# Kernel optimization log

Measured on AMD Instinct MI355X. Metric: run time of the kernel, lower is better.

The kernel has to match this reference:

```python
import jax, jax.numpy as jnp
import numpy as np

HIDDEN = 1024
HEADS = 16
HEAD_DIM = HIDDEN // HEADS
LN_EPS = 1e-5


def setup_inputs() -> dict:
    key = jax.random.key(0)
    ks = jax.random.split(key, 8)
    B, S = 4, 2048
    s = 1.0 / np.sqrt(HIDDEN)
    return {
        "x": jax.random.normal(ks[0], (B, S, HIDDEN), dtype=jnp.float32),
        "Wq": jax.random.normal(ks[1], (HIDDEN, HIDDEN), dtype=jnp.float32) * s,
        "bq": jax.random.normal(ks[2], (HIDDEN,), dtype=jnp.float32) * 0.01,
        "Wk": jax.random.normal(ks[3], (HIDDEN, HIDDEN), dtype=jnp.float32) * s,
        "bk": jax.random.normal(ks[4], (HIDDEN,), dtype=jnp.float32) * 0.01,
        "Wv": jax.random.normal(ks[5], (HIDDEN, HIDDEN), dtype=jnp.float32) * s,
        "bv": jax.random.normal(ks[6], (HIDDEN,), dtype=jnp.float32) * 0.01,
        "gamma": jnp.ones((HIDDEN,), dtype=jnp.float32),
        "beta": jnp.zeros((HIDDEN,), dtype=jnp.float32),
    }


def reference(x, Wq, bq, Wk, bk, Wv, bv, gamma, beta):
    B, S, H = x.shape
    # LayerNorm
    mu = jnp.mean(x, axis=-1, keepdims=True)
    var = jnp.mean(jnp.square(x - mu), axis=-1, keepdims=True)
    xn = (x - mu) / jnp.sqrt(var + LN_EPS) * gamma + beta
    # QKV projections -> [B, heads, S, head_dim]
    def split_heads(t):
        return t.reshape(B, S, HEADS, HEAD_DIM).transpose(0, 2, 1, 3)
    q = split_heads(xn @ Wq + bq)
    k = split_heads(xn @ Wk + bk)
    v = split_heads(xn @ Wv + bv)
    scores = jnp.einsum("bhqd,bhkd->bhqk", q, k) / np.sqrt(HEAD_DIM)
    probs = jax.nn.softmax(scores, axis=-1)
    attended = jnp.einsum("bhqk,bhkd->bhqd", probs, v)
    attended = attended.transpose(0, 2, 1, 3).reshape(B, S, H)
    # residual (dropout = 0.0 / eval mode is identity)
    return xn + attended
```

## Files before the change

kernel.cpp:

```cpp
#include <hip/hip_runtime.h>
#include <hip/hip_bf16.h>

#define HIDDEN 1024
#define HEADS 16
#define HEAD_DIM 64
#define SEQ 2048
#define BATCH 4

typedef __attribute__((ext_vector_type(8))) short bf16x8;
typedef __attribute__((ext_vector_type(4))) float f32x4;
typedef __attribute__((ext_vector_type(16))) float f32x16;
typedef __attribute__((ext_vector_type(4))) short short4v;

static __device__ __forceinline__ unsigned short f2bf(float f) {
  union { float f; unsigned u; } u;
  u.f = f;
  unsigned r = u.u + 0x7fffu + ((u.u >> 16) & 1u);
  return (unsigned short)(r >> 16);
}

static __device__ __forceinline__ unsigned packtr(float lo, float hi) {
  union { float f; unsigned u; } a, b;
  a.f = lo; b.f = hi;
#if __has_builtin(__builtin_amdgcn_perm)
  return __builtin_amdgcn_perm(b.u, a.u, 0x07060302u);
#else
  return (b.u & 0xFFFF0000u) | (a.u >> 16);
#endif
}

static __device__ __forceinline__ bf16x8 frag4(unsigned u0, unsigned u1,
                                               unsigned u2, unsigned u3) {
  union { unsigned u[4]; bf16x8 v; } t;
  t.u[0] = u0; t.u[1] = u1; t.u[2] = u2; t.u[3] = u3;
  return t.v;
}

static __device__ __forceinline__ float fexp2(float x) {
#if __has_builtin(__builtin_amdgcn_exp2f)
  return __builtin_amdgcn_exp2f(x);
#else
  return exp2f(x);
#endif
}

typedef const __attribute__((address_space(1))) unsigned int* gp1_t;
typedef __attribute__((address_space(3))) unsigned int* lp3_t;
static __device__ __forceinline__ void gload_lds16(const void* g, void* l) {
  __builtin_amdgcn_global_load_lds((gp1_t)g, (lp3_t)l, 16, 0, 0);
}

__global__ __launch_bounds__(256) void wtrans_kernel(
    const float* __restrict__ Wq, const float* __restrict__ Wk,
    const float* __restrict__ Wv, unsigned short* __restrict__ Wt) {
  __shared__ float tile[64][65];
  int z = blockIdx.z;
  const float* W = (z == 0) ? Wq : (z == 1) ? Wk : Wv;
  int k0 = blockIdx.x * 64, n0 = blockIdx.y * 64;
  int tid = threadIdx.x;
  int tr = tid >> 4;
  int tc = tid & 15;
#pragma unroll
  for (int p = 0; p < 4; ++p) {
    int kk = p * 16 + tr;
    float4 v = *(const float4*)(W + (size_t)(k0 + kk) * HIDDEN + n0 + tc * 4);
    tile[kk][tc * 4 + 0] = v.x; tile[kk][tc * 4 + 1] = v.y;
    tile[kk][tc * 4 + 2] = v.z; tile[kk][tc * 4 + 3] = v.w;
  }
  __syncthreads();
  unsigned short* op = Wt + (size_t)z * HIDDEN * HIDDEN;
#pragma unroll
  for (int p = 0; p < 4; ++p) {
    int nn = p * 16 + tr;
    short4v o;
    o.x = (short)f2bf(tile[tc * 4 + 0][nn]);
    o.y = (short)f2bf(tile[tc * 4 + 1][nn]);
    o.z = (short)f2bf(tile[tc * 4 + 2][nn]);
    o.w = (short)f2bf(tile[tc * 4 + 3][nn]);
    *(short4v*)(op + (size_t)(n0 + nn) * HIDDEN + k0 + tc * 4) = o;
  }
}

__global__ __launch_bounds__(256) void ln_kernel(
    const float* __restrict__ x, const float* __restrict__ gamma,
    const float* __restrict__ beta, float* __restrict__ out,
    unsigned short* __restrict__ xnb) {
  int row = blockIdx.x;
  int tid = threadIdx.x;
  const float4* xr = (const float4*)(x + (size_t)row * HIDDEN);
  float4 v = xr[tid];
  float s = v.x + v.y + v.z + v.w;
  float sq = v.x * v.x + v.y * v.y + v.z * v.z + v.w * v.w;
#pragma unroll
  for (int off = 32; off >= 1; off >>= 1) {
    s += __shfl_xor(s, off);
    sq += __shfl_xor(sq, off);
  }
  __shared__ float red[8];
  int wave = tid >> 6, lane = tid & 63;
  if (lane == 0) { red[wave] = s; red[4 + wave] = sq; }
  __syncthreads();
  s = red[0] + red[1] + red[2] + red[3];
  sq = red[4] + red[5] + red[6] + red[7];
  float mu = s * (1.0f / HIDDEN);
  float var = sq * (1.0f / HIDDEN) - mu * mu;
  float rstd = rsqrtf(var + 1e-5f);
  float4 g = ((const float4*)gamma)[tid];
  float4 bt = ((const float4*)beta)[tid];
  float4 o;
  o.x = (v.x - mu) * rstd * g.x + bt.x;
  o.y = (v.y - mu) * rstd * g.y + bt.y;
  o.z = (v.z - mu) * rstd * g.z + bt.z;
  o.w = (v.w - mu) * rstd * g.w + bt.w;
  ((float4*)(out + (size_t)row * HIDDEN))[tid] = o;
  short4v p;
  p.x = (short)f2bf(o.x); p.y = (short)f2bf(o.y);
  p.z = (short)f2bf(o.z); p.w = (short)f2bf(o.w);
  *((short4v*)(xnb + (size_t)row * HIDDEN) + tid) = p;
}

__global__ __launch_bounds__(256) void qkv_gemm(
    const unsigned short* __restrict__ xnb, const unsigned short* __restrict__ Wt,
    const float* __restrict__ bq, const float* __restrict__ bk,
    const float* __restrict__ bv, unsigned short* __restrict__ qO,
    unsigned short* __restrict__ kO, unsigned short* __restrict__ vtO) {
  __shared__ unsigned short As[128 * 64];
  __shared__ unsigned short Bs[128 * 64];
  int z = blockIdx.z;
  int m0 = blockIdx.x * 128;
  int n0 = blockIdx.y * 128;
  int tid = threadIdx.x;
  int wave = tid >> 6, lane = tid & 63;
  int lr = lane & 15, g = lane >> 4;
  int wm = wave >> 1, wn = wave & 1;
  const unsigned short* Ab = xnb + (size_t)m0 * HIDDEN;
  const unsigned short* Bb = Wt + (size_t)z * HIDDEN * HIDDEN + (size_t)n0 * HIDDEN;
  int srow = wave * 8 + (lane >> 3);
  int scol = ((lane & 7) ^ (lane >> 3)) << 3;
  f32x4 acc[4][4];
#pragma unroll
  for (int i = 0; i < 4; ++i)
#pragma unroll
    for (int j = 0; j < 4; ++j) acc[i][j] = (f32x4){0.f, 0.f, 0.f, 0.f};

#pragma unroll 1
  for (int k0 = 0; k0 < HIDDEN; k0 += 64) {
#pragma unroll
    for (int i = 0; i < 4; ++i) {
      int row = i * 32 + srow;
      gload_lds16(Ab + (size_t)row * HIDDEN + k0 + scol, &As[(i * 32 + wave * 8) * 64]);
      gload_lds16(Bb + (size_t)row * HIDDEN + k0 + scol, &Bs[(i * 32 + wave * 8) * 64]);
    }
    __syncthreads();
    bf16x8 aF[4][2], bF[4][2];
#pragma unroll
    for (int mb = 0; mb < 4; ++mb) {
      int row = wm * 64 + mb * 16 + lr;
#pragma unroll
      for (int ks = 0; ks < 2; ++ks)
        aF[mb][ks] = *(const bf16x8*)&As[row * 64 + (((ks * 4 + g) ^ (row & 7)) << 3)];
    }
#pragma unroll
    for (int nb = 0; nb < 4; ++nb) {
      int row = wn * 64 + nb * 16 + lr;
#pragma unroll
      for (int ks = 0; ks < 2; ++ks)
        bF[nb][ks] = *(const bf16x8*)&Bs[row * 64 + (((ks * 4 + g) ^ (row & 7)) << 3)];
    }
#pragma unroll
    for (int ks = 0; ks < 2; ++ks)
#pragma unroll
      for (int mb = 0; mb < 4; ++mb)
#pragma unroll
        for (int nb = 0; nb < 4; ++nb)
          acc[mb][nb] = __builtin_amdgcn_mfma_f32_16x16x32_bf16(aF[mb][ks], bF[nb][ks], acc[mb][nb], 0, 0, 0);
    __syncthreads();
  }
  const float* bias = (z == 0) ? bq : (z == 1) ? bk : bv;
  if (z == 2) {
#pragma unroll
    for (int nb = 0; nb < 4; ++nb) {
      int n = n0 + wn * 64 + nb * 16 + lr;
      float bsv = bias[n];
      int h = n >> 6, d = n & 63;
#pragma unroll
      for (int mb = 0; mb < 4; ++mb) {
        int m = m0 + wm * 64 + mb * 16 + g * 4;
        int bb = m >> 11, sIdx = m & 2047;
        short4v pk;
        pk.x = (short)f2bf(acc[mb][nb][0] + bsv);
        pk.y = (short)f2bf(acc[mb][nb][1] + bsv);
        pk.z = (short)f2bf(acc[mb][nb][2] + bsv);
        pk.w = (short)f2bf(acc[mb][nb][3] + bsv);
        *(short4v*)(vtO + (size_t)((bb * HEADS + h) * HEAD_DIM + d) * SEQ + sIdx) = pk;
      }
    }
  } else {
    unsigned short* outp = (z == 0) ? qO : kO;
    float scale = (z == 0) ? 0.18033688011112042f : 1.0f;
#pragma unroll
    for (int nb = 0; nb < 4; ++nb) {
      int n = n0 + wn * 64 + nb * 16 + lr;
      float bsv = bias[n];
      int h = n >> 6, d = n & 63;
#pragma unroll
      for (int mb = 0; mb < 4; ++mb) {
#pragma unroll
        for (int r = 0; r < 4; ++r) {
          int m = m0 + wm * 64 + mb * 16 + g * 4 + r;
          int bb = m >> 11, sIdx = m & 2047;
          unsigned short bits = f2bf((acc[mb][nb][r] + bsv) * scale);
          outp[(size_t)((bb * HEADS + h) * SEQ + sIdx) * HEAD_DIM + d] = bits;
        }
      }
    }
  }
}

static __device__ __forceinline__ void attn_subtile(
    const unsigned short* __restrict__ Kb, const unsigned short* __restrict__ Vb,
    const int (&koff)[4], const bf16x8 (&qF)[4],
    const f32x16& ZERO, f32x16& o0, f32x16& o1, float& lsum) {
  f32x16 sc0, sc1;
  __builtin_amdgcn_s_setprio(1);
  {
    bf16x8 k0 = *(const bf16x8*)&Kb[koff[0]];
    bf16x8 k1 = *(const bf16x8*)&Kb[koff[0] + 2048];
    sc0 = __builtin_amdgcn_mfma_f32_32x32x16_bf16(k0, qF[0], ZERO, 0, 0, 0);
    sc1 = __builtin_amdgcn_mfma_f32_32x32x16_bf16(k1, qF[0], ZERO, 0, 0, 0);
  }
#pragma unroll
  for (int s = 1; s < 4; ++s) {
    bf16x8 k0 = *(const bf16x8*)&Kb[koff[s]];
    bf16x8 k1 = *(const bf16x8*)&Kb[koff[s] + 2048];
    sc0 = __builtin_amdgcn_mfma_f32_32x32x16_bf16(k0, qF[s], sc0, 0, 0, 0);
    sc1 = __builtin_amdgcn_mfma_f32_32x32x16_bf16(k1, qF[s], sc1, 0, 0, 0);
  }
  __builtin_amdgcn_s_setprio(0);
#pragma unroll
  for (int s = 0; s < 4; ++s) {
    float e[8];
#pragma unroll
    for (int j = 0; j < 8; ++j) {
      float scv = (s < 2) ? sc0[8 * s + j] : sc1[8 * (s - 2) + j];
      e[j] = fexp2(scv);
    }
    lsum += ((e[0] + e[1]) + (e[2] + e[3])) + ((e[4] + e[5]) + (e[6] + e[7]));
    unsigned pa0 = packtr(e[0], e[1]);
    unsigned pb0 = packtr(e[2], e[3]);
    unsigned pa1 = packtr(e[4], e[5]);
    unsigned pb1 = packtr(e[6], e[7]);
#if __has_builtin(__builtin_amdgcn_permlane32_swap)
    auto ra = __builtin_amdgcn_permlane32_swap(pa0, pa1, false, false);
    auto rb = __builtin_amdgcn_permlane32_swap(pb0, pb1, false, false);
    bf16x8 pF = frag4(ra[0], rb[0], ra[1], rb[1]);
#else
    int hf = (threadIdx.x & 63) >> 5;
    unsigned t0 = __shfl_xor(hf ? pa0 : pa1, 32);
    unsigned t1 = __shfl_xor(hf ? pb0 : pb1, 32);
    bf16x8 pF = frag4(hf ? t0 : pa0, hf ? t1 : pb0,
                      hf ? pa1 : t0, hf ? pb1 : t1);
#endif
    bf16x8 v0 = *(const bf16x8*)&Vb[koff[s]];
    bf16x8 v1 = *(const bf16x8*)&Vb[koff[s] + 2048];
    __builtin_amdgcn_s_setprio(1);
    o0 = __builtin_amdgcn_mfma_f32_32x32x16_bf16(v0, pF, o0, 0, 0, 0);
    o1 = __builtin_amdgcn_mfma_f32_32x32x16_bf16(v1, pF, o1, 0, 0, 0);
    __builtin_amdgcn_s_setprio(0);
  }
}

__global__ __launch_bounds__(512, 4) void attn_kernel(
    const unsigned short* __restrict__ qB, const unsigned short* __restrict__ kB,
    const unsigned short* __restrict__ vtB, float* __restrict__ out) {
  __shared__ unsigned short Kt[2][2][64 * 64];
  __shared__ unsigned short Vt[2][2][64 * 64];
  int orig = blockIdx.y * gridDim.x + blockIdx.x;
  int swz = (orig & 7) * 64 + (orig >> 3);
  int bx = swz & 7;
  int by = swz >> 3;
  int b = by >> 4, hh = by & 15;
  int tid = threadIdx.x, wave = tid >> 6, lane = tid & 63;
  int lq = lane & 31;
  int hf = lane >> 5;
  int q0 = bx * 256 + wave * 32;
  const unsigned short* qh = qB + (size_t)by * SEQ * HEAD_DIM;
  const unsigned short* kh = kB + (size_t)by * SEQ * HEAD_DIM;
  const unsigned short* vh = vtB + (size_t)by * HEAD_DIM * SEQ;

  bf16x8 qF[4];
#pragma unroll
  for (int s = 0; s < 4; ++s)
    qF[s] = *(const bf16x8*)(qh + (size_t)(q0 + lq) * HEAD_DIM + s * 16 + hf * 8);

  int srow = wave * 8 + (lane >> 3);
  int scoff = ((lane & 7) ^ (lane >> 3)) << 3;
  int xorb = (lq & 7) << 4;
  int koff[4];
#pragma unroll
  for (int s = 0; s < 4; ++s)
    koff[s] = (lq * 128 + ((s * 32 + hf * 16) ^ xorb)) >> 1;

  f32x16 o0, o1, ZERO;
#pragma unroll
  for (int r = 0; r < 16; ++r) { o0[r] = 0.f; o1[r] = 0.f; ZERO[r] = 0.f; }
  float lsum = 0.f;

#pragma unroll
  for (int sub = 0; sub < 2; ++sub) {
    gload_lds16(kh + (size_t)(sub * 64 + srow) * HEAD_DIM + scoff, &Kt[0][sub][wave * 512]);
    gload_lds16(vh + (size_t)srow * SEQ + sub * 64 + scoff, &Vt[0][sub][wave * 512]);
  }
  __syncthreads();

#pragma unroll 1
  for (int t = 0; t < 16; ++t) {
    int cur = t & 1;
    if (t < 15) {
      int kv1 = (t + 1) * 128;
#pragma unroll
      for (int sub = 0; sub < 2; ++sub) {
        gload_lds16(kh + (size_t)(kv1 + sub * 64 + srow) * HEAD_DIM + scoff,
                    &Kt[cur ^ 1][sub][wave * 512]);
        gload_lds16(vh + (size_t)srow * SEQ + kv1 + sub * 64 + scoff,
                    &Vt[cur ^ 1][sub][wave * 512]);
      }
    }
    attn_subtile(Kt[cur][0], Vt[cur][0], koff, qF, ZERO, o0, o1, lsum);
    attn_subtile(Kt[cur][1], Vt[cur][1], koff, qF, ZERO, o0, o1, lsum);
    __syncthreads();
  }
  lsum += __shfl_xor(lsum, 32);
  float inv = 1.0f / lsum;
  float* orow = out + ((size_t)b * SEQ + q0 + lq) * HIDDEN + hh * HEAD_DIM;
#pragma unroll
  for (int r = 0; r < 16; ++r) {
    int d0 = (r & 3) + 8 * (r >> 2) + 4 * hf;
    orow[d0] += o0[r] * inv;
    orow[32 + d0] += o1[r] * inv;
  }
}

extern "C" void kernel_launch(void* const* d_in, const int* in_sizes, int n_in,
                              void* d_out, int out_size, void* d_ws, size_t ws_size,
                              hipStream_t stream) {
  const float* x     = (const float*)d_in[0];
  const float* Wq    = (const float*)d_in[1];
  const float* bq    = (const float*)d_in[2];
  const float* Wk    = (const float*)d_in[3];
  const float* bk    = (const float*)d_in[4];
  const float* Wv    = (const float*)d_in[5];
  const float* bv    = (const float*)d_in[6];
  const float* gamma = (const float*)d_in[7];
  const float* beta  = (const float*)d_in[8];
  float* out = (float*)d_out;
  char* ws = (char*)d_ws;
  const size_t MB = 1024 * 1024;
  unsigned short* xnb = (unsigned short*)(ws);
  unsigned short* Wt  = (unsigned short*)(ws + 16 * MB);
  unsigned short* qb  = (unsigned short*)(ws + 22 * MB);
  unsigned short* kb  = (unsigned short*)(ws + 38 * MB);
  unsigned short* vtb = (unsigned short*)(ws + 54 * MB);

  hipLaunchKernelGGL(wtrans_kernel, dim3(16, 16, 3), dim3(256), 0, stream, Wq, Wk, Wv, Wt);
  hipLaunchKernelGGL(ln_kernel, dim3(BATCH * SEQ), dim3(256), 0, stream, x, gamma, beta, out, xnb);
  hipLaunchKernelGGL(qkv_gemm, dim3(64, 8, 3), dim3(256), 0, stream, xnb, Wt, bq, bk, bv, qb, kb, vtb);
  hipLaunchKernelGGL(attn_kernel, dim3(8, 64), dim3(512), 0, stream, qb, kb, vtb, out);
}
```

Baseline: 174.4 us.

## Double-buffer QKV GEMM tiles and re-layout attention K/V LDS tiles

The QKV GEMM now keeps two LDS buffers for the A and B tiles and prefetches the next k-slice while computing on the current one, so global loads can overlap with MFMA work. The attention kernel also changes how K and V tiles are staged into LDS: each wave loads an 8-element column chunk for all 64 rows, replacing the XOR-swizzled row layout, and fragment offsets are recomputed to match. The aim is fewer load stalls and simpler LDS addressing, at the cost of doubling GEMM LDS use, which may lower occupancy. The new attention global loads are more strided and may have different LDS bank-conflict behaviour.

```diff
diff --git a/kernel.cpp b/kernel.cpp
--- a/kernel.cpp
+++ b/kernel.cpp
@@ -124,8 +124,8 @@
     const float* __restrict__ bq, const float* __restrict__ bk,
     const float* __restrict__ bv, unsigned short* __restrict__ qO,
     unsigned short* __restrict__ kO, unsigned short* __restrict__ vtO) {
-  __shared__ unsigned short As[128 * 64];
-  __shared__ unsigned short Bs[128 * 64];
+  __shared__ unsigned short As[2][128 * 64];
+  __shared__ unsigned short Bs[2][128 * 64];
   int z = blockIdx.z;
   int m0 = blockIdx.x * 128;
   int n0 = blockIdx.y * 128;
@@ -143,29 +143,40 @@
 #pragma unroll
     for (int j = 0; j < 4; ++j) acc[i][j] = (f32x4){0.f, 0.f, 0.f, 0.f};
 
+#pragma unroll
+  for (int i = 0; i < 4; ++i) {
+    int row = i * 32 + srow;
+    gload_lds16(Ab + (size_t)row * HIDDEN + scol, &As[0][(i * 32 + wave * 8) * 64]);
+    gload_lds16(Bb + (size_t)row * HIDDEN + scol, &Bs[0][(i * 32 + wave * 8) * 64]);
+  }
+  __syncthreads();
+
 #pragma unroll 1
-  for (int k0 = 0; k0 < HIDDEN; k0 += 64) {
-#pragma unroll
-    for (int i = 0; i < 4; ++i) {
-      int row = i * 32 + srow;
-      gload_lds16(Ab + (size_t)row * HIDDEN + k0 + scol, &As[(i * 32 + wave * 8) * 64]);
-      gload_lds16(Bb + (size_t)row * HIDDEN + k0 + scol, &Bs[(i * 32 + wave * 8) * 64]);
-    }
-    __syncthreads();
+  for (int t = 0; t < 16; ++t) {
+    int cur = t & 1;
+    if (t < 15) {
+      int k1 = (t + 1) * 64;
+#pragma unroll
+      for (int i = 0; i < 4; ++i) {
+        int row = i * 32 + srow;
+        gload_lds16(Ab + (size_t)row * HIDDEN + k1 + scol, &As[cur ^ 1][(i * 32 + wave * 8) * 64]);
+        gload_lds16(Bb + (size_t)row * HIDDEN + k1 + scol, &Bs[cur ^ 1][(i * 32 + wave * 8) * 64]);
+      }
+    }
     bf16x8 aF[4][2], bF[4][2];
 #pragma unroll
     for (int mb = 0; mb < 4; ++mb) {
       int row = wm * 64 + mb * 16 + lr;
 #pragma unroll
       for (int ks = 0; ks < 2; ++ks)
-        aF[mb][ks] = *(const bf16x8*)&As[row * 64 + (((ks * 4 + g) ^ (row & 7)) << 3)];
+        aF[mb][ks] = *(const bf16x8*)&As[cur][row * 64 + (((ks * 4 + g) ^ (row & 7)) << 3)];
     }
 #pragma unroll
     for (int nb = 0; nb < 4; ++nb) {
       int row = wn * 64 + nb * 16 + lr;
 #pragma unroll
       for (int ks = 0; ks < 2; ++ks)
-        bF[nb][ks] = *(const bf16x8*)&Bs[row * 64 + (((ks * 4 + g) ^ (row & 7)) << 3)];
+        bF[nb][ks] = *(const bf16x8*)&Bs[cur][row * 64 + (((ks * 4 + g) ^ (row & 7)) << 3)];
     }
 #pragma unroll
     for (int ks = 0; ks < 2; ++ks)
@@ -225,14 +236,14 @@
   __builtin_amdgcn_s_setprio(1);
   {
     bf16x8 k0 = *(const bf16x8*)&Kb[koff[0]];
-    bf16x8 k1 = *(const bf16x8*)&Kb[koff[0] + 2048];
+    bf16x8 k1 = *(const bf16x8*)&Kb[koff[0] + 256];
     sc0 = __builtin_amdgcn_mfma_f32_32x32x16_bf16(k0, qF[0], ZERO, 0, 0, 0);
     sc1 = __builtin_amdgcn_mfma_f32_32x32x16_bf16(k1, qF[0], ZERO, 0, 0, 0);
   }
 #pragma unroll
   for (int s = 1; s < 4; ++s) {
     bf16x8 k0 = *(const bf16x8*)&Kb[koff[s]];
-    bf16x8 k1 = *(const bf16x8*)&Kb[koff[s] + 2048];
+    bf16x8 k1 = *(const bf16x8*)&Kb[koff[s] + 256];
     sc0 = __builtin_amdgcn_mfma_f32_32x32x16_bf16(k0, qF[s], sc0, 0, 0, 0);
     sc1 = __builtin_amdgcn_mfma_f32_32x32x16_bf16(k1, qF[s], sc1, 0, 0, 0);
   }
@@ -262,7 +273,7 @@
                       hf ? pa1 : t0, hf ? pb1 : t1);
 #endif
     bf16x8 v0 = *(const bf16x8*)&Vb[koff[s]];
-    bf16x8 v1 = *(const bf16x8*)&Vb[koff[s] + 2048];
+    bf16x8 v1 = *(const bf16x8*)&Vb[koff[s] + 256];
     __builtin_amdgcn_s_setprio(1);
     o0 = __builtin_amdgcn_mfma_f32_32x32x16_bf16(v0, pF, o0, 0, 0, 0);
     o1 = __builtin_amdgcn_mfma_f32_32x32x16_bf16(v1, pF, o1, 0, 0, 0);
@@ -293,13 +304,10 @@
   for (int s = 0; s < 4; ++s)
     qF[s] = *(const bf16x8*)(qh + (size_t)(q0 + lq) * HEAD_DIM + s * 16 + hf * 8);
 
-  int srow = wave * 8 + (lane >> 3);
-  int scoff = ((lane & 7) ^ (lane >> 3)) << 3;
-  int xorb = (lq & 7) << 4;
   int koff[4];
 #pragma unroll
   for (int s = 0; s < 4; ++s)
-    koff[s] = (lq * 128 + ((s * 32 + hf * 16) ^ xorb)) >> 1;
+    koff[s] = (2 * s + hf) * 512 + lq * 8;
 
   f32x16 o0, o1, ZERO;
 #pragma unroll
@@ -308,8 +316,8 @@
 
 #pragma unroll
   for (int sub = 0; sub < 2; ++sub) {
-    gload_lds16(kh + (size_t)(sub * 64 + srow) * HEAD_DIM + scoff, &Kt[0][sub][wave * 512]);
-    gload_lds16(vh + (size_t)srow * SEQ + sub * 64 + scoff, &Vt[0][sub][wave * 512]);
+    gload_lds16(kh + (size_t)(sub * 64 + lane) * HEAD_DIM + wave * 8, &Kt[0][sub][wave * 512]);
+    gload_lds16(vh + (size_t)lane * SEQ + sub * 64 + wave * 8, &Vt[0][sub][wave * 512]);
   }
   __syncthreads();
 
@@ -320,9 +328,9 @@
       int kv1 = (t + 1) * 128;
 #pragma unroll
       for (int sub = 0; sub < 2; ++sub) {
-        gload_lds16(kh + (size_t)(kv1 + sub * 64 + srow) * HEAD_DIM + scoff,
+        gload_lds16(kh + (size_t)(kv1 + sub * 64 + lane) * HEAD_DIM + wave * 8,
                     &Kt[cur ^ 1][sub][wave * 512]);
-        gload_lds16(vh + (size_t)srow * SEQ + kv1 + sub * 64 + scoff,
+        gload_lds16(vh + (size_t)lane * SEQ + kv1 + sub * 64 + wave * 8,
                     &Vt[cur ^ 1][sub][wave * 512]);
       }
     }
```

Measured after the change: 167.5 us. -3.9%, faster.
